# Optimization experiments

Measured on AMD Instinct MI355X. Metric: run time of the kernel, lower is better.

Reference implementation:

```python
import jax, jax.numpy as jnp
import numpy as np

NUM_NODES = 40000
NUM_EDGES = 400000
DIM = 128
NUM_REL = 502  # num_relation * 2
NUM_HEAD = 1


def setup_inputs() -> dict:
    key = jax.random.key(0)
    ks = jax.random.split(key, 16)
    d = DIM
    return {
        "curr_stat": jax.random.normal(ks[0], (NUM_NODES, d), jnp.float32),
        "last_stat": jax.random.normal(ks[1], (NUM_NODES, d), jnp.float32),
        "relemb_weight": jax.random.normal(ks[2], (NUM_REL, d), jnp.float32),
        "selfrel_weight": jax.random.normal(ks[3], (1, d), jnp.float32),
        "Wq": jax.random.normal(ks[4], (2 * d, d), jnp.float32) * (1.0 / np.sqrt(2 * d)),
        "bq": jax.random.normal(ks[5], (d,), jnp.float32) * 0.02,
        "Wk": jax.random.normal(ks[6], (2 * d, d), jnp.float32) * (1.0 / np.sqrt(2 * d)),
        "bk": jax.random.normal(ks[7], (d,), jnp.float32) * 0.02,
        "Wv": jax.random.normal(ks[8], (d, d), jnp.float32) * (1.0 / np.sqrt(d)),
        "bv": jax.random.normal(ks[9], (d,), jnp.float32) * 0.02,
        "dyn_weight": jax.random.normal(ks[10], (d, d), jnp.float32) * (1.0 / np.sqrt(d)),
        "edge_index": jax.random.randint(ks[11], (2, NUM_EDGES), 0, NUM_NODES, jnp.int32),
        "edge_type": jax.random.randint(ks[12], (NUM_EDGES,), 0, NUM_REL, jnp.int32),
    }


def _segment_softmax(scores, seg, num_segments):
    # scores: [E, H]; softmax over edges sharing the same destination segment
    m = jax.ops.segment_max(scores, seg, num_segments=num_segments)  # [N, H]
    e = jnp.exp(scores - m[seg])
    s = jax.ops.segment_sum(e, seg, num_segments=num_segments)  # [N, H]
    return e / s[seg]


def reference(curr_stat, last_stat, relemb_weight, selfrel_weight,
              Wq, bq, Wk, bk, Wv, bv, dyn_weight,
              edge_index, edge_type):
    N, D = curr_stat.shape
    H = NUM_HEAD
    HD = D // H

    # append self-loop edges for every node, with the dedicated self-relation
    loop = jnp.arange(N, dtype=edge_index.dtype)
    src = jnp.concatenate([edge_index[0], loop])  # [E_total]
    dst = jnp.concatenate([edge_index[1], loop])  # [E_total]
    type_emb = jnp.concatenate(
        [relemb_weight[edge_type], jnp.broadcast_to(selfrel_weight, (N, D))], axis=0)

    E = src.shape[0]
    # linear projections (x @ W + b); torch Linear stores W transposed, same math
    q = (jnp.concatenate([curr_stat[dst], type_emb], -1) @ Wq + bq).reshape(E, H, HD)
    k = (jnp.concatenate([last_stat[src], type_emb], -1) @ Wk + bk).reshape(E, H, HD)
    v = (last_stat[src] @ Wv + bv).reshape(E, H, HD)

    attn = jnp.sum(q * k, axis=-1) / np.sqrt(HD).astype(np.float32)  # [E, H]

    dyn_prob = _segment_softmax(attn, dst, N)   # [E, H]
    sta_prob = _segment_softmax(-attn, dst, N)  # [E, H]

    counts = jax.ops.segment_sum(jnp.ones((E,), jnp.float32), dst, num_segments=N)
    denom = jnp.maximum(counts, 1.0)[:, None]  # scatter-mean denominator

    feat_dyn = jax.ops.segment_sum((dyn_prob[..., None] * v).reshape(E, D), dst,
                                   num_segments=N) / denom
    feat_sta = jax.ops.segment_sum((sta_prob[..., None] * v).reshape(E, D), dst,
                                   num_segments=N) / denom

    # stack (feat_sta, feat_dyn @ dyn_weight) -> [2, N, D]
    return jnp.stack([feat_sta, feat_dyn @ dyn_weight])
```

## Files before the change

kernel.cpp:

```cpp
#include <hip/hip_runtime.h>
#include <hip/hip_bf16.h>
#include <math.h>

#define DIMC 128
#define CS2L (0.08838834764831845f * 1.4426950408889634f)

typedef __attribute__((ext_vector_type(8))) short short8;
typedef __attribute__((ext_vector_type(4))) float floatx4;
typedef __attribute__((ext_vector_type(2))) float f32x2;

static __device__ __forceinline__ unsigned pk2(float lo, float hi) {
    __hip_bfloat162 h = __float22bfloat162_rn(make_float2(lo, hi));
    return *(unsigned*)&h;
}
static __device__ __forceinline__ unsigned short f2bf(float x) {
    union { float f; unsigned int u; } v; v.f = x;
    unsigned int r = v.u + 0x7FFFu + ((v.u >> 16) & 1u);
    return (unsigned short)(r >> 16);
}
static __device__ __forceinline__ f32x2 bfp(unsigned int u) {
    union { unsigned int i; float f; } a, b;
    a.i = u << 16; b.i = u & 0xFFFF0000u;
    f32x2 r; r.x = a.f; r.y = b.f; return r;
}

template<int CTRL>
static __device__ __forceinline__ float dpp_add(float x) {
    int y = __builtin_amdgcn_update_dpp(0, __float_as_int(x), CTRL, 0xF, 0xF, true);
    return x + __int_as_float(y);
}
static __device__ __forceinline__ float red8(float p) {
    p = dpp_add<0xB1>(p);
    p = dpp_add<0x4E>(p);
    p = dpp_add<0x141>(p);
    return p;
}

struct PrepArgs {
    const float* W[6];
    unsigned short* F[6];
    float wscale[6];
    const float* relemb; const float* selfrel;
    float* TypeEmb;
    int* deg;
    int R; int N;
};

__global__ __launch_bounds__(64) void prep_all(PrepArgs a)
{
    int b = blockIdx.x;
    int lane = threadIdx.x;
    if (b < 192) {
        int mat = b >> 5, ts = b & 31;
        int s = ts & 3, t = ts >> 2;
        int q = lane >> 4, c = lane & 15;
        const float* W = a.W[mat];
        float sc = a.wscale[mat];
        unsigned short o[8];
        #pragma unroll
        for (int j = 0; j < 8; ++j)
            o[j] = f2bf(W[(long)(s * 32 + q * 8 + j) * DIMC + t * 16 + c] * sc);
        uint4 u;
        u.x = (unsigned)o[0] | ((unsigned)o[1] << 16);
        u.y = (unsigned)o[2] | ((unsigned)o[3] << 16);
        u.z = (unsigned)o[4] | ((unsigned)o[5] << 16);
        u.w = (unsigned)o[6] | ((unsigned)o[7] << 16);
        ((uint4*)a.F[mat])[ts * 64 + lane] = u;
    } else if (b < 192 + a.R + 1) {
        int r = b - 192;
        const float* src = (r < a.R) ? (a.relemb + (long)r * DIMC) : a.selfrel;
        float2 v = ((const float2*)src)[lane];
        ((float2*)(a.TypeEmb + (long)r * DIMC))[lane] = v;
    } else {
        int i = (b - (192 + a.R + 1)) * 64 + lane;
        if (i < a.N) a.deg[i] = 0;
    }
}

struct GemmM5 {
    const float*          Af[5];
    const unsigned short* Ab[5];
    const unsigned short* F[5];
    const float*          bias[5];
    float                 bscale[5];
    float*                outf[5];
    unsigned short*       outb[5];
    int                   ostride[5];
    int                   ooff[5];
    int                   M[5];
    const unsigned short* F2;
    const float*          bias2;
    unsigned short*       outb2;
    const int*            hist_dst;
    int*                  hist_deg;
    int                   hist_E;
};

__global__ __launch_bounds__(256) void gemm_mfma(GemmM5 g)
{
    __shared__ uint4 wlds[2048];

    if (blockIdx.y == 4) {
        int i = blockIdx.x * blockDim.x + threadIdx.x;
        int stride = gridDim.x * blockDim.x;
        for (; i < g.hist_E; i += stride) atomicAdd(&g.hist_deg[g.hist_dst[i]], 1);
        return;
    }

    const int wave = threadIdx.x >> 6;
    const int lane = threadIdx.x & 63;
    const int q = lane >> 4, c = lane & 15;

    if (blockIdx.y == 1) {
        const int M = g.M[1];
        if ((int)blockIdx.x * 64 >= M) return;
        const int rowbase = blockIdx.x * 64 + wave * 16;

        {
            const uint4* Fp = (const uint4*)g.F[1];
            #pragma unroll
            for (int j = 0; j < 8; ++j)
                wlds[threadIdx.x + j * 256] = Fp[threadIdx.x + j * 256];
        }
        int rowA = rowbase + c; if (rowA > M - 1) rowA = M - 1;
        short8 af[4];
        {
            const float* Ar = g.Af[1] + (long)rowA * DIMC + q * 8;
            #pragma unroll
            for (int s = 0; s < 4; ++s) {
                float4 x0 = *(const float4*)(Ar + s * 32);
                float4 x1 = *(const float4*)(Ar + s * 32 + 4);
                uint4 u;
                u.x = pk2(x0.x, x0.y);
                u.y = pk2(x0.z, x0.w);
                u.z = pk2(x1.x, x1.y);
                u.w = pk2(x1.z, x1.w);
                af[s] = *(short8*)&u;
            }
        }
        floatx4 acc[8];
        #pragma unroll
        for (int t = 0; t < 8; ++t) acc[t] = (floatx4){0.f, 0.f, 0.f, 0.f};
        __syncthreads();
        #pragma unroll
        for (int t = 0; t < 8; ++t)
            #pragma unroll
            for (int s = 0; s < 4; ++s) {
                uint4 u = wlds[(t * 4 + s) * 64 + lane];
                acc[t] = __builtin_amdgcn_mfma_f32_16x16x32_bf16(af[s], *(short8*)&u, acc[t], 0, 0, 0);
            }
        __syncthreads();
        {
            const uint4* Fp = (const uint4*)g.F2;
            #pragma unroll
            for (int j = 0; j < 8; ++j)
                wlds[threadIdx.x + j * 256] = Fp[threadIdx.x + j * 256];
        }
        #pragma unroll
        for (int t = 0; t < 8; ++t)
            #pragma unroll
            for (int r = 0; r < 4; ++r) {
                float other = __shfl_xor(acc[t][r], 1);
                int row = rowbase + q * 4 + r;
                if ((lane & 1) == 0 && row < M)
                    ((unsigned*)g.outb[1])[(long)row * 64 + t * 8 + (c >> 1)] = pk2(acc[t][r], other);
            }
        #pragma unroll
        for (int t = 0; t < 8; ++t) {
            float b = g.bias2[t * 16 + c];
            acc[t] = (floatx4){b, b, b, b};
        }
        __syncthreads();
        #pragma unroll
        for (int t = 0; t < 8; ++t)
            #pragma unroll
            for (int s = 0; s < 4; ++s) {
                uint4 u = wlds[(t * 4 + s) * 64 + lane];
                acc[t] = __builtin_amdgcn_mfma_f32_16x16x32_bf16(af[s], *(short8*)&u, acc[t], 0, 0, 0);
            }
        #pragma unroll
        for (int t = 0; t < 8; ++t)
            #pragma unroll
            for (int r = 0; r < 4; ++r) {
                float other = __shfl_xor(acc[t][r], 1);
                int row = rowbase + q * 4 + r;
                if ((lane & 1) == 0 && row < M)
                    ((unsigned*)g.outb2)[(long)row * 64 + t * 8 + (c >> 1)] = pk2(acc[t][r], other);
            }
        return;
    }

    const int which = blockIdx.y;
    const int M = g.M[which];
    if ((int)blockIdx.x * 64 >= M) return;

    const float*          __restrict__ Af   = g.Af[which];
    const unsigned short* __restrict__ Ab   = g.Ab[which];
    const unsigned short* __restrict__ F    = g.F[which];
    const float*          __restrict__ bias = g.bias[which];
    const float bsc = g.bscale[which];
    float*          __restrict__ outf = g.outf[which];
    unsigned short* __restrict__ outb = g.outb[which];
    const int ostride = g.ostride[which];
    const int ooff    = g.ooff[which];
    const int rowbase = blockIdx.x * 64 + wave * 16;

    {
        const uint4* Fp = (const uint4*)F;
        #pragma unroll
        for (int j = 0; j < 8; ++j)
            wlds[threadIdx.x + j * 256] = Fp[threadIdx.x + j * 256];
    }

    int rowA = rowbase + c; if (rowA > M - 1) rowA = M - 1;
    short8 af[4];
    if (Af) {
        const float* Ar = Af + (long)rowA * DIMC + q * 8;
        #pragma unroll
        for (int s = 0; s < 4; ++s) {
            float4 x0 = *(const float4*)(Ar + s * 32);
            float4 x1 = *(const float4*)(Ar + s * 32 + 4);
            uint4 u;
            u.x = pk2(x0.x, x0.y);
            u.y = pk2(x0.z, x0.w);
            u.z = pk2(x1.x, x1.y);
            u.w = pk2(x1.z, x1.w);
            af[s] = *(short8*)&u;
        }
    } else {
        const unsigned short* Ar = Ab + (long)rowA * DIMC + q * 8;
        #pragma unroll
        for (int s = 0; s < 4; ++s) {
            uint4 u = *(const uint4*)(Ar + s * 32);
            af[s] = *(short8*)&u;
        }
    }

    floatx4 acc[8];
    #pragma unroll
    for (int t = 0; t < 8; ++t) {
        float b = bias ? bias[t * 16 + c] * bsc : 0.0f;
        acc[t] = (floatx4){b, b, b, b};
    }

    __syncthreads();

    #pragma unroll
    for (int t = 0; t < 8; ++t)
        #pragma unroll
        for (int s = 0; s < 4; ++s) {
            uint4 u = wlds[(t * 4 + s) * 64 + lane];
            acc[t] = __builtin_amdgcn_mfma_f32_16x16x32_bf16(af[s], *(short8*)&u, acc[t], 0, 0, 0);
        }

    if (outf) {
        #pragma unroll
        for (int t = 0; t < 8; ++t)
            #pragma unroll
            for (int r = 0; r < 4; ++r) {
                int row = rowbase + q * 4 + r;
                if (row < M)
                    outf[(long)row * DIMC + t * 16 + c] = acc[t][r];
            }
    } else {
        #pragma unroll
        for (int t = 0; t < 8; ++t)
            #pragma unroll
            for (int r = 0; r < 4; ++r) {
                float other = __shfl_xor(acc[t][r], 1);
                int row = rowbase + q * 4 + r;
                if ((lane & 1) == 0 && row < M) {
                    unsigned word = pk2(acc[t][r], other);
                    ((unsigned*)outb)[((long)row * 64 + t * 8 + (c >> 1))
                                      * (long)ostride + ooff] = word;
                }
            }
    }
}

__global__ __launch_bounds__(256) void partial_sums(const int* __restrict__ deg,
                                                    int* __restrict__ partial, int N)
{
    __shared__ int sh[256];
    int t = threadIdx.x;
    int beg = blockIdx.x * 1024 + t * 4;
    int s = 0;
    if (beg + 3 < N) { int4 v = *(const int4*)(deg + beg); s = v.x + v.y + v.z + v.w; }
    else { for (int j = 0; j < 4; ++j) if (beg + j < N) s += deg[beg + j]; }
    sh[t] = s;
    __syncthreads();
    for (int d = 128; d >= 1; d >>= 1) {
        if (t < d) sh[t] += sh[t + d];
        __syncthreads();
    }
    if (t == 0) partial[blockIdx.x] = sh[0];
}

__global__ __launch_bounds__(256) void scan_write_offsets(const int* __restrict__ deg,
                                                          const int* __restrict__ partial,
                                                          int* __restrict__ offs,
                                                          int* __restrict__ cursor, int N, int nb)
{
    __shared__ int sh[256];
    __shared__ int sbase;
    int t = threadIdx.x;
    if (t < 64) {
        int v = (t < nb && t < (int)blockIdx.x) ? partial[t] : 0;
        #pragma unroll
        for (int d = 32; d >= 1; d >>= 1) v += __shfl_xor(v, d);
        if (t == 0) sbase = v;
    }
    int beg = blockIdx.x * 1024 + t * 4;
    int d0 = 0, d1 = 0, d2 = 0, d3 = 0;
    if (beg + 3 < N) { int4 v = *(const int4*)(deg + beg); d0 = v.x; d1 = v.y; d2 = v.z; d3 = v.w; }
    else {
        if (beg < N)     d0 = deg[beg];
        if (beg + 1 < N) d1 = deg[beg + 1];
        if (beg + 2 < N) d2 = deg[beg + 2];
        if (beg + 3 < N) d3 = deg[beg + 3];
    }
    int s = d0 + d1 + d2 + d3;
    sh[t] = s;
    __syncthreads();
    for (int d = 1; d < 256; d <<= 1) {
        int v = (t >= d) ? sh[t - d] : 0;
        __syncthreads();
        sh[t] += v;
        __syncthreads();
    }
    int base = sbase + sh[t] - s;
    int o0 = base, o1 = o0 + d0, o2 = o1 + d1, o3 = o2 + d2;
    if (beg < N)     { offs[beg]     = o0; cursor[beg]     = o0; }
    if (beg + 1 < N) { offs[beg + 1] = o1; cursor[beg + 1] = o1; }
    if (beg + 2 < N) { offs[beg + 2] = o2; cursor[beg + 2] = o2; }
    if (beg + 3 < N) { offs[beg + 3] = o3; cursor[beg + 3] = o3; }
}

__global__ void scatter_kernel(const int* __restrict__ src, const int* __restrict__ dst,
                               const int* __restrict__ etype, int* __restrict__ cursor,
                               int2* __restrict__ sedge, int E)
{
    int e = blockIdx.x * blockDim.x + threadIdx.x;
    if (e < E) {
        int d = dst[e];
        int p = atomicAdd(&cursor[d], 1);
        sedge[p] = make_int2(src[e] << 8, etype[e] << 9);
    }
}

__global__ __launch_bounds__(256) void node_kernel(
    const char*  __restrict__ Qb,
    const char*  __restrict__ Kb,
    const char*  __restrict__ Vb,
    const char*  __restrict__ QKb,
    const int* __restrict__ offs, const int* __restrict__ deg,
    const int2* __restrict__ sedge,
    float* __restrict__ out_sta, uint4* __restrict__ feat_dyn,
    int N, int R)
{
    int n = (blockIdx.x * blockDim.x + threadIdx.x) >> 6;
    int lane = threadIdx.x & 63;
    if (n >= N) return;
    const int el = lane & 7;
    const int g8 = lane >> 3;
    const int ko = el << 5;
    const int qo = el << 6;

    int base = offs[n];
    int dcnt = deg[n];
    int etot = dcnt + 1;

    f32x2 qr[8];
    {
        const uint4* qp = (const uint4*)(Qb + ((long)n << 8) + ko);
        uint4 w0 = qp[0], w1 = qp[1];
        qr[0] = bfp(w0.x); qr[1] = bfp(w0.y); qr[2] = bfp(w0.z); qr[3] = bfp(w0.w);
        qr[4] = bfp(w1.x); qr[5] = bfp(w1.y); qr[6] = bfp(w1.z); qr[7] = bfp(w1.w);
    }

    float s_d = 0.0f, s_s = 0.0f;
    f32x2 ad[8], as_[8];
    #pragma unroll
    for (int j = 0; j < 8; ++j) { ad[j] = (f32x2){0.f, 0.f}; as_[j] = ad[j]; }

    const int selfK = n << 8, selfQ = R << 9;

    int T = (etot + 7) >> 3;
    for (int it = 0; it < T; ++it) {
        int i = 8 * it + g8;
        bool vv = i < etot;
        bool re = i < dcnt;
        int2 e = re ? sedge[base + i] : make_int2(selfK, selfQ);

        uint4 k0 = *(const uint4*)(Kb + e.x + ko);
        uint4 k1 = *(const uint4*)(Kb + e.x + ko + 16);
        uint4 v0 = *(const uint4*)(Vb + e.x + ko);
        uint4 v1 = *(const uint4*)(Vb + e.x + ko + 16);
        uint4 qA = *(const uint4*)(QKb + e.y + qo);
        uint4 qB = *(const uint4*)(QKb + e.y + qo + 16);
        uint4 qC = *(const uint4*)(QKb + e.y + qo + 32);
        uint4 qD = *(const uint4*)(QKb + e.y + qo + 48);

        f32x2 dp;
        dp  = (qr[0] + bfp(qA.x)) * (bfp(k0.x) + bfp(qA.y));
        dp += (qr[1] + bfp(qA.z)) * (bfp(k0.y) + bfp(qA.w));
        dp += (qr[2] + bfp(qB.x)) * (bfp(k0.z) + bfp(qB.y));
        dp += (qr[3] + bfp(qB.z)) * (bfp(k0.w) + bfp(qB.w));
        dp += (qr[4] + bfp(qC.x)) * (bfp(k1.x) + bfp(qC.y));
        dp += (qr[5] + bfp(qC.z)) * (bfp(k1.y) + bfp(qC.w));
        dp += (qr[6] + bfp(qD.x)) * (bfp(k1.z) + bfp(qD.y));
        dp += (qr[7] + bfp(qD.z)) * (bfp(k1.w) + bfp(qD.w));
        float p = red8(dp.x + dp.y);

        float wd = vv ? exp2f(p)  : 0.0f;
        float ws = vv ? exp2f(-p) : 0.0f;
        s_d += wd; s_s += ws;

        f32x2 vp[8];
        vp[0] = bfp(v0.x); vp[1] = bfp(v0.y); vp[2] = bfp(v0.z); vp[3] = bfp(v0.w);
        vp[4] = bfp(v1.x); vp[5] = bfp(v1.y); vp[6] = bfp(v1.z); vp[7] = bfp(v1.w);
        #pragma unroll
        for (int j = 0; j < 8; ++j) {
            ad[j]  += vp[j] * wd;
            as_[j] += vp[j] * ws;
        }
    }

    #define MRG(x) { x += __shfl_xor(x, 8); x += __shfl_xor(x, 16); x += __shfl_xor(x, 32); }
    MRG(s_d) MRG(s_s)
    #pragma unroll
    for (int j = 0; j < 8; ++j) {
        MRG(ad[j].x)  MRG(ad[j].y)
        MRG(as_[j].x) MRG(as_[j].y)
    }
    #undef MRG

    if (g8 == 0) {
        float denom = (float)(dcnt + 1);
        float id_ = 1.0f / (s_d * denom);
        float is_ = 1.0f / (s_s * denom);
        float4* op = (float4*)(out_sta + (long)n * DIMC + el * 16);
        op[0] = make_float4(as_[0].x * is_, as_[0].y * is_, as_[1].x * is_, as_[1].y * is_);
        op[1] = make_float4(as_[2].x * is_, as_[2].y * is_, as_[3].x * is_, as_[3].y * is_);
        op[2] = make_float4(as_[4].x * is_, as_[4].y * is_, as_[5].x * is_, as_[5].y * is_);
        op[3] = make_float4(as_[6].x * is_, as_[6].y * is_, as_[7].x * is_, as_[7].y * is_);
        uint4 w0, w1;
        w0.x = pk2(ad[0].x * id_, ad[0].y * id_);
        w0.y = pk2(ad[1].x * id_, ad[1].y * id_);
        w0.z = pk2(ad[2].x * id_, ad[2].y * id_);
        w0.w = pk2(ad[3].x * id_, ad[3].y * id_);
        w1.x = pk2(ad[4].x * id_, ad[4].y * id_);
        w1.y = pk2(ad[5].x * id_, ad[5].y * id_);
        w1.z = pk2(ad[6].x * id_, ad[6].y * id_);
        w1.w = pk2(ad[7].x * id_, ad[7].y * id_);
        feat_dyn[(unsigned)n * 16u + el * 2]     = w0;
        feat_dyn[(unsigned)n * 16u + el * 2 + 1] = w1;
    }
}

extern "C" void kernel_launch(void* const* d_in, const int* in_sizes, int n_in,
                              void* d_out, int out_size, void* d_ws, size_t ws_size,
                              hipStream_t stream)
{
    const float* curr    = (const float*)d_in[0];
    const float* last    = (const float*)d_in[1];
    const float* relemb  = (const float*)d_in[2];
    const float* selfrel = (const float*)d_in[3];
    const float* Wq      = (const float*)d_in[4];
    const float* bq      = (const float*)d_in[5];
    const float* Wk      = (const float*)d_in[6];
    const float* bk      = (const float*)d_in[7];
    const float* Wv      = (const float*)d_in[8];
    const float* bv      = (const float*)d_in[9];
    const float* dynw    = (const float*)d_in[10];
    const int*   eidx    = (const int*)d_in[11];
    const int*   etype   = (const int*)d_in[12];
    float* out = (float*)d_out;

    const int N = in_sizes[0] / DIMC;
    const int E = in_sizes[12];
    const int R = in_sizes[2] / DIMC;
    const int* esrc = eidx;
    const int* edst = eidx + E;

    char* wp = (char*)d_ws;
    auto alloc = [&](size_t bytes) { char* r = wp; wp += (bytes + 15) & ~(size_t)15; return r; };
    size_t nd = (size_t)N * DIMC;
    unsigned short* Qb    = (unsigned short*)alloc((size_t)N * 256);
    unsigned short* Kb    = (unsigned short*)alloc((size_t)N * 256);
    unsigned short* Vb    = (unsigned short*)alloc((size_t)N * 256);
    unsigned short* Fdb   = (unsigned short*)alloc(nd * 2);
    uint4*          QKre  = (uint4*)alloc((size_t)(R + 1) * 32 * 16);
    float*          TypeEmb = (float*)alloc((size_t)(R + 2) * DIMC * 4);
    unsigned short* FW[6];
    for (int m = 0; m < 6; ++m) FW[m] = (unsigned short*)alloc(2048 * 8 * 2);
    int*            deg   = (int*)alloc((size_t)N * 4);
    int*            offs  = (int*)alloc((size_t)N * 4);
    int*            cursor= (int*)alloc((size_t)N * 4);
    int2*           sedge = (int2*)alloc((size_t)E * 8);
    int*            partial = (int*)alloc(256 * 4);

    const int gblk = N / 64;
    const int sblk = (N + 1023) / 1024;

    PrepArgs pa;
    pa.W[0] = Wq;   pa.W[1] = Wk;   pa.W[2] = Wv;
    pa.W[3] = dynw; pa.W[4] = Wq + (size_t)DIMC * DIMC; pa.W[5] = Wk + (size_t)DIMC * DIMC;
    pa.wscale[0] = CS2L; pa.wscale[1] = 1.0f; pa.wscale[2] = 1.0f;
    pa.wscale[3] = 1.0f; pa.wscale[4] = CS2L; pa.wscale[5] = 1.0f;
    for (int m = 0; m < 6; ++m) pa.F[m] = FW[m];
    pa.relemb = relemb; pa.selfrel = selfrel; pa.TypeEmb = TypeEmb;
    pa.deg = deg; pa.R = R; pa.N = N;
    int pgrid = 192 + (R + 1) + (N + 63) / 64;
    hipLaunchKernelGGL(prep_all, dim3(pgrid), dim3(64), 0, stream, pa);

    GemmM5 g5;
    for (int s = 0; s < 5; ++s) { g5.Af[s] = nullptr; g5.Ab[s] = nullptr; g5.outf[s] = nullptr; g5.outb[s] = nullptr; g5.bias[s] = nullptr; g5.bscale[s] = 1.0f; g5.ostride[s] = 1; g5.ooff[s] = 0; g5.M[s] = 0; }
    g5.Af[0] = curr;    g5.F[0] = FW[0]; g5.outb[0] = Qb;  g5.M[0] = N;
    g5.Af[1] = last;    g5.F[1] = FW[1]; g5.outb[1] = Kb;  g5.M[1] = N;
    g5.F2 = FW[2]; g5.bias2 = bv; g5.outb2 = Vb;
    g5.Af[2] = TypeEmb; g5.F[2] = FW[4]; g5.bias[2] = bq;  g5.outb[2] = (unsigned short*)QKre;
    g5.ostride[2] = 2;  g5.ooff[2] = 0;  g5.M[2] = R + 1;  g5.bscale[2] = CS2L;
    g5.Af[3] = TypeEmb; g5.F[3] = FW[5]; g5.bias[3] = bk;  g5.outb[3] = (unsigned short*)QKre;
    g5.ostride[3] = 2;  g5.ooff[3] = 1;  g5.M[3] = R + 1;
    g5.hist_dst = edst; g5.hist_deg = deg; g5.hist_E = E;
    hipLaunchKernelGGL(gemm_mfma, dim3(gblk, 5), dim3(256), 0, stream, g5);

    hipLaunchKernelGGL(partial_sums, dim3(sblk), dim3(256), 0, stream, deg, partial, N);
    hipLaunchKernelGGL(scan_write_offsets, dim3(sblk), dim3(256), 0, stream,
                       deg, partial, offs, cursor, N, sblk);
    hipLaunchKernelGGL(scatter_kernel, dim3((E + 255) / 256), dim3(256), 0, stream,
                       esrc, edst, etype, cursor, sedge, E);

    hipLaunchKernelGGL(node_kernel, dim3((N + 3) / 4), dim3(256), 0, stream,
                       (const char*)Qb, (const char*)Kb, (const char*)Vb, (const char*)QKre,
                       offs, deg, sedge, out, (uint4*)Fdb, N, R);

    GemmM5 gf;
    for (int s = 0; s < 5; ++s) { gf.Af[s] = nullptr; gf.Ab[s] = nullptr; gf.outf[s] = nullptr; gf.outb[s] = nullptr; gf.bias[s] = nullptr; gf.bscale[s] = 1.0f; gf.ostride[s] = 1; gf.ooff[s] = 0; gf.M[s] = 0; }
    gf.Ab[0] = Fdb; gf.F[0] = FW[3]; gf.outf[0] = out + nd; gf.M[0] = N;
    gf.F2 = FW[2]; gf.bias2 = bv; gf.outb2 = Vb;
    gf.hist_dst = edst; gf.hist_deg = deg; gf.hist_E = 0;
    hipLaunchKernelGGL(gemm_mfma, dim3(gblk, 1), dim3(256), 0, stream, gf);
}
```

Measured before the change: 248.7 us.

## Remap node kernel lanes: 32 lanes per edge, two edges per wave

Changes the per-node wavefront mapping from 8 edges × 8 lanes (16 dims each) to 2 edges × 32 lanes (4 dims each). Each lane now does narrower loads and keeps far fewer registers. The dot-product reduction grows to 32 lanes using DPP plus one shuffle, and the final cross-group merge shrinks to a single xor-32 shuffle. This is meant to raise occupancy and cut the merge epilogue, at the cost of more loop iterations per node and a longer reduction per edge.

Measured after the change: 215.4 us. -13.4%, faster.

```diff
diff --git a/kernel.cpp b/kernel.cpp
--- a/kernel.cpp
+++ b/kernel.cpp
@@ -29,10 +29,11 @@
     int y = __builtin_amdgcn_update_dpp(0, __float_as_int(x), CTRL, 0xF, 0xF, true);
     return x + __int_as_float(y);
 }
-static __device__ __forceinline__ float red8(float p) {
+static __device__ __forceinline__ float red16(float p) {
     p = dpp_add<0xB1>(p);
     p = dpp_add<0x4E>(p);
     p = dpp_add<0x141>(p);
+    p = dpp_add<0x140>(p);
     return p;
 }
 
@@ -355,106 +356,77 @@
     const char*  __restrict__ QKb,
     const int* __restrict__ offs, const int* __restrict__ deg,
     const int2* __restrict__ sedge,
-    float* __restrict__ out_sta, uint4* __restrict__ feat_dyn,
+    float* __restrict__ out_sta, uint2* __restrict__ feat_dyn,
     int N, int R)
 {
     int n = (blockIdx.x * blockDim.x + threadIdx.x) >> 6;
     int lane = threadIdx.x & 63;
     if (n >= N) return;
-    const int el = lane & 7;
-    const int g8 = lane >> 3;
-    const int ko = el << 5;
-    const int qo = el << 6;
+    const int ql = lane & 31;
+    const int h  = lane >> 5;
+    const int lo8  = ql << 3;
+    const int lo16 = ql << 4;
 
     int base = offs[n];
     int dcnt = deg[n];
     int etot = dcnt + 1;
 
-    f32x2 qr[8];
+    f32x2 q01, q23;
     {
-        const uint4* qp = (const uint4*)(Qb + ((long)n << 8) + ko);
-        uint4 w0 = qp[0], w1 = qp[1];
-        qr[0] = bfp(w0.x); qr[1] = bfp(w0.y); qr[2] = bfp(w0.z); qr[3] = bfp(w0.w);
-        qr[4] = bfp(w1.x); qr[5] = bfp(w1.y); qr[6] = bfp(w1.z); qr[7] = bfp(w1.w);
+        uint2 qw = *(const uint2*)(Qb + ((long)n << 8) + lo8);
+        q01 = bfp(qw.x);
+        q23 = bfp(qw.y);
     }
 
     float s_d = 0.0f, s_s = 0.0f;
-    f32x2 ad[8], as_[8];
-    #pragma unroll
-    for (int j = 0; j < 8; ++j) { ad[j] = (f32x2){0.f, 0.f}; as_[j] = ad[j]; }
+    f32x2 accd0 = {0.f, 0.f}, accd1 = accd0;
+    f32x2 accs0 = accd0, accs1 = accd0;
 
     const int selfK = n << 8, selfQ = R << 9;
 
-    int T = (etot + 7) >> 3;
+    int T = (etot + 1) >> 1;
     for (int it = 0; it < T; ++it) {
-        int i = 8 * it + g8;
+        int i = 2 * it + h;
         bool vv = i < etot;
         bool re = i < dcnt;
         int2 e = re ? sedge[base + i] : make_int2(selfK, selfQ);
 
-        uint4 k0 = *(const uint4*)(Kb + e.x + ko);
-        uint4 k1 = *(const uint4*)(Kb + e.x + ko + 16);
-        uint4 v0 = *(const uint4*)(Vb + e.x + ko);
-        uint4 v1 = *(const uint4*)(Vb + e.x + ko + 16);
-        uint4 qA = *(const uint4*)(QKb + e.y + qo);
-        uint4 qB = *(const uint4*)(QKb + e.y + qo + 16);
-        uint4 qC = *(const uint4*)(QKb + e.y + qo + 32);
-        uint4 qD = *(const uint4*)(QKb + e.y + qo + 48);
-
-        f32x2 dp;
-        dp  = (qr[0] + bfp(qA.x)) * (bfp(k0.x) + bfp(qA.y));
-        dp += (qr[1] + bfp(qA.z)) * (bfp(k0.y) + bfp(qA.w));
-        dp += (qr[2] + bfp(qB.x)) * (bfp(k0.z) + bfp(qB.y));
-        dp += (qr[3] + bfp(qB.z)) * (bfp(k0.w) + bfp(qB.w));
-        dp += (qr[4] + bfp(qC.x)) * (bfp(k1.x) + bfp(qC.y));
-        dp += (qr[5] + bfp(qC.z)) * (bfp(k1.y) + bfp(qC.w));
-        dp += (qr[6] + bfp(qD.x)) * (bfp(k1.z) + bfp(qD.y));
-        dp += (qr[7] + bfp(qD.z)) * (bfp(k1.w) + bfp(qD.w));
-        float p = red8(dp.x + dp.y);
-
-        float wd = vv ? exp2f(p)  : 0.0f;
-        float ws = vv ? exp2f(-p) : 0.0f;
+        uint2 kx  = *(const uint2*)(Kb + e.x + lo8);
+        uint2 vx  = *(const uint2*)(Vb + e.x + lo8);
+        uint4 qk  = *(const uint4*)(QKb + e.y + lo16);
+
+        f32x2 a0 = q01 + bfp(qk.x), a1 = q23 + bfp(qk.z);
+        f32x2 k0 = bfp(kx.x) + bfp(qk.y), k1 = bfp(kx.y) + bfp(qk.w);
+        f32x2 dp = a0 * k0;
+        dp += a1 * k1;
+        float pd = dp.x + dp.y;
+        pd = red16(pd);
+        pd += __shfl_xor(pd, 16);
+
+        float wd = vv ? exp2f(pd)  : 0.0f;
+        float ws = vv ? exp2f(-pd) : 0.0f;
         s_d += wd; s_s += ws;
 
-        f32x2 vp[8];
-        vp[0] = bfp(v0.x); vp[1] = bfp(v0.y); vp[2] = bfp(v0.z); vp[3] = bfp(v0.w);
-        vp[4] = bfp(v1.x); vp[5] = bfp(v1.y); vp[6] = bfp(v1.z); vp[7] = bfp(v1.w);
-        #pragma unroll
-        for (int j = 0; j < 8; ++j) {
-            ad[j]  += vp[j] * wd;
-            as_[j] += vp[j] * ws;
-        }
-    }
-
-    #define MRG(x) { x += __shfl_xor(x, 8); x += __shfl_xor(x, 16); x += __shfl_xor(x, 32); }
-    MRG(s_d) MRG(s_s)
-    #pragma unroll
-    for (int j = 0; j < 8; ++j) {
-        MRG(ad[j].x)  MRG(ad[j].y)
-        MRG(as_[j].x) MRG(as_[j].y)
-    }
-    #undef MRG
-
-    if (g8 == 0) {
+        f32x2 v0 = bfp(vx.x), v1 = bfp(vx.y);
+        accd0 += v0 * wd; accd1 += v1 * wd;
+        accs0 += v0 * ws; accs1 += v1 * ws;
+    }
+
+    s_d += __shfl_xor(s_d, 32);
+    s_s += __shfl_xor(s_s, 32);
+    accd0.x += __shfl_xor(accd0.x, 32); accd0.y += __shfl_xor(accd0.y, 32);
+    accd1.x += __shfl_xor(accd1.x, 32); accd1.y += __shfl_xor(accd1.y, 32);
+    accs0.x += __shfl_xor(accs0.x, 32); accs0.y += __shfl_xor(accs0.y, 32);
+    accs1.x += __shfl_xor(accs1.x, 32); accs1.y += __shfl_xor(accs1.y, 32);
+
+    if (h == 0) {
         float denom = (float)(dcnt + 1);
         float id_ = 1.0f / (s_d * denom);
         float is_ = 1.0f / (s_s * denom);
-        float4* op = (float4*)(out_sta + (long)n * DIMC + el * 16);
-        op[0] = make_float4(as_[0].x * is_, as_[0].y * is_, as_[1].x * is_, as_[1].y * is_);
-        op[1] = make_float4(as_[2].x * is_, as_[2].y * is_, as_[3].x * is_, as_[3].y * is_);
-        op[2] = make_float4(as_[4].x * is_, as_[4].y * is_, as_[5].x * is_, as_[5].y * is_);
-        op[3] = make_float4(as_[6].x * is_, as_[6].y * is_, as_[7].x * is_, as_[7].y * is_);
-        uint4 w0, w1;
-        w0.x = pk2(ad[0].x * id_, ad[0].y * id_);
-        w0.y = pk2(ad[1].x * id_, ad[1].y * id_);
-        w0.z = pk2(ad[2].x * id_, ad[2].y * id_);
-        w0.w = pk2(ad[3].x * id_, ad[3].y * id_);
-        w1.x = pk2(ad[4].x * id_, ad[4].y * id_);
-        w1.y = pk2(ad[5].x * id_, ad[5].y * id_);
-        w1.z = pk2(ad[6].x * id_, ad[6].y * id_);
-        w1.w = pk2(ad[7].x * id_, ad[7].y * id_);
-        feat_dyn[(unsigned)n * 16u + el * 2]     = w0;
-        feat_dyn[(unsigned)n * 16u + el * 2 + 1] = w1;
+        ((float4*)(out_sta + (long)n * DIMC))[ql] =
+            make_float4(accs0.x * is_, accs0.y * is_, accs1.x * is_, accs1.y * is_);
+        feat_dyn[(unsigned)n * 32u + ql] =
+            make_uint2(pk2(accd0.x * id_, accd0.y * id_), pk2(accd1.x * id_, accd1.y * id_));
     }
 }
 
@@ -534,7 +506,7 @@
 
     hipLaunchKernelGGL(node_kernel, dim3((N + 3) / 4), dim3(256), 0, stream,
                        (const char*)Qb, (const char*)Kb, (const char*)Vb, (const char*)QKre,
-                       offs, deg, sedge, out, (uint4*)Fdb, N, R);
+                       offs, deg, sedge, out, (uint2*)Fdb, N, R);
 
     GemmM5 gf;
     for (int s = 0; s < 5; ++s) { gf.Af[s] = nullptr; gf.Ab[s] = nullptr; gf.outf[s] = nullptr; gf.outb[s] = nullptr; gf.bias[s] = nullptr; gf.bscale[s] = 1.0f; gf.ostride[s] = 1; gf.ooff[s] = 0; gf.M[s] = 0; }
```
